# Performance work log

Hardware: AMD Instinct MI355X
Metric: run time of the kernel (lower is better)

## Reference

```python
import jax, jax.numpy as jnp
import numpy as np

N_NODES = 100000
N_EDGES = 1600000
N_GRAPHS = 64
HID = 128
N_EXPERTS = 8
IN_DIM = 4


def setup_inputs() -> dict:
    key = jax.random.key(0)
    ks = jax.random.split(key, 12)
    atomic_numbers = jax.random.uniform(ks[0], (N_NODES,), dtype=jnp.float32) * 80.0
    pos = jax.random.normal(ks[1], (N_NODES, 3), dtype=jnp.float32)
    edge_index = jax.random.randint(ks[2], (2, N_EDGES), 0, N_NODES, dtype=jnp.int64)
    batch = jnp.sort(jax.random.randint(ks[3], (N_NODES,), 0, N_GRAPHS, dtype=jnp.int64))
    s1 = 1.0 / np.sqrt(IN_DIM)
    s2 = 1.0 / np.sqrt(HID)
    W1 = jax.random.uniform(ks[4], (IN_DIM, HID), jnp.float32, -s1, s1)
    b1 = jnp.zeros((HID,), jnp.float32)
    W2 = jax.random.uniform(ks[5], (HID, HID), jnp.float32, -s2, s2)
    b2 = jnp.zeros((HID,), jnp.float32)
    Wlin = jax.random.uniform(ks[6], (HID, N_EXPERTS), jnp.float32, -s2, s2)
    blin = jax.random.uniform(ks[7], (N_EXPERTS,), jnp.float32, -s2, s2)
    return {"atomic_numbers": atomic_numbers, "pos": pos, "edge_index": edge_index,
            "batch": batch, "W1": W1, "b1": b1, "W2": W2, "b2": b2,
            "Wlin": Wlin, "blin": blin}


def _gcn_conv(x, W, b, src, dst, deg_inv_sqrt, n_nodes):
    # PyG GCNConv: x' = W x; aggregate deg^-1/2[src]*deg^-1/2[dst] * x'[src] into dst; + bias
    h = x @ W  # [N, out]
    norm = deg_inv_sqrt[src] * deg_inv_sqrt[dst]  # [E+N]
    msg = h[src] * norm[:, None]  # gathered, normalized messages
    out = jax.ops.segment_sum(msg, dst, num_segments=n_nodes)
    return out + b


def reference(atomic_numbers, pos, edge_index, batch, W1, b1, W2, b2, Wlin, blin):
    n = atomic_numbers.shape[0]
    x = jnp.concatenate([atomic_numbers[:, None], pos], axis=-1)  # [N, 4]
    # add self-loops (GCNConv default add_self_loops=True)
    loop = jnp.arange(n, dtype=edge_index.dtype)
    src = jnp.concatenate([edge_index[0], loop])
    dst = jnp.concatenate([edge_index[1], loop])
    deg = jax.ops.segment_sum(jnp.ones_like(dst, dtype=jnp.float32), dst, num_segments=n)
    deg_inv_sqrt = jnp.where(deg > 0, jax.lax.rsqrt(jnp.maximum(deg, 1e-12)), 0.0)
    x = _gcn_conv(x, W1, b1, src, dst, deg_inv_sqrt, n)
    x = jax.nn.relu(x)
    # dropout p=0.5 is identity in eval mode
    x = _gcn_conv(x, W2, b2, src, dst, deg_inv_sqrt, n)
    x = x @ Wlin + blin  # [N, num_experts]
    # global_mean_pool over graph ids
    sums = jax.ops.segment_sum(x, batch, num_segments=N_GRAPHS)
    cnts = jax.ops.segment_sum(jnp.ones((n,), jnp.float32), batch, num_segments=N_GRAPHS)
    pooled = sums / jnp.maximum(cnts, 1.0)[:, None]
    return jax.nn.log_softmax(pooled, axis=1)
```

## Files before the change

### kernel.cpp

```cpp
#include <hip/hip_runtime.h>
#include <math.h>

#define HID 128
#define NEXP 8
#define NGRAPH 64
#define EPC 6144
#define MAXB 512
#define NXC 8
#define NREP 8
#define NPS 8
#define HALF 128

__device__ inline unsigned short f2bf(float f) {
    unsigned u = __float_as_uint(f);
    u += 0x7FFF + ((u >> 16) & 1);
    return (unsigned short)(u >> 16);
}
__device__ inline unsigned packbf(float lo, float hi) {
    return (unsigned)f2bf(lo) | ((unsigned)f2bf(hi) << 16);
}
__device__ inline float bflo(unsigned u) { return __uint_as_float(u << 16); }
__device__ inline float bfhi(unsigned u) { return __uint_as_float(u & 0xFFFF0000u); }

__global__ void k_init0(float* __restrict__ pool, float* __restrict__ pcnt,
                        const float* __restrict__ W2, const float* __restrict__ Wlin,
                        const float* __restrict__ b2, float* __restrict__ C,
                        float* __restrict__ bb2, int* __restrict__ gcur8,
                        int mregions, int capx) {
    int i = blockIdx.x * 256 + threadIdx.x;
    if (i < mregions) gcur8[i] = i * capx;
    if (i < NREP * NGRAPH * NEXP) pool[i] = 0.0f;
    if (i < NREP * NGRAPH) pcnt[i] = 0.0f;
    int ci = i - NREP * NGRAPH * NEXP;
    if (ci >= 0 && ci < HID * NEXP) {
        int k = ci >> 3, j = ci & 7;
        float s = 0.0f;
        for (int m = 0; m < HID; m++) s += W2[k * HID + m] * Wlin[m * NEXP + j];
        C[ci] = s;
    }
    int bi = ci - HID * NEXP;
    if (bi >= 0 && bi < NEXP) {
        float s = 0.0f;
        for (int m = 0; m < HID; m++) s += b2[m] * Wlin[m * NEXP + bi];
        bb2[bi] = s;
    }
}

__global__ void __launch_bounds__(256) k_binA(
        const int* __restrict__ src, const int* __restrict__ dst,
        int* __restrict__ gcur8, unsigned* __restrict__ binned, int e, int nbuck) {
    __shared__ int h0[MAXB];
    __shared__ int h1[MAXB];
    __shared__ int lstart[MAXB];
    __shared__ int lcur[MAXB];
    __shared__ int gbase[MAXB];
    __shared__ int wtot[4];
    __shared__ unsigned packed[EPC];
    __shared__ unsigned short sbkt[EPC];
    int c = blockIdx.x, t = threadIdx.x;
    int w = t >> 6, lane = t & 63;
    int x = c & (NXC - 1);
    int start = c * EPC;
    int m = e - start < EPC ? e - start : EPC;

    int d[24], sv[24];
    if (m == EPC) {
        const int4* d4 = (const int4*)(dst + start);
        const int4* s4 = (const int4*)(src + start);
#pragma unroll
        for (int q = 0; q < 6; q++) {
            int4 dd4 = d4[6 * t + q];
            int4 ss4 = s4[6 * t + q];
            d[4 * q + 0] = dd4.x; d[4 * q + 1] = dd4.y;
            d[4 * q + 2] = dd4.z; d[4 * q + 3] = dd4.w;
            sv[4 * q + 0] = ss4.x; sv[4 * q + 1] = ss4.y;
            sv[4 * q + 2] = ss4.z; sv[4 * q + 3] = ss4.w;
        }
    } else {
#pragma unroll
        for (int j = 0; j < 24; j++) {
            int idx = t * 24 + j;
            if (idx < m) { d[j] = dst[start + idx]; sv[j] = src[start + idx]; }
        }
    }
    int* hm = (w < 2) ? h0 : h1;
    h0[t] = 0; h0[t + 256] = 0;
    h1[t] = 0; h1[t + 256] = 0;
    __syncthreads();
#pragma unroll
    for (int j = 0; j < 24; j++)
        if (t * 24 + j < m) atomicAdd(&hm[d[j] >> 8], 1);
    __syncthreads();
    int v0 = h0[2 * t] + h1[2 * t];
    int v1 = h0[2 * t + 1] + h1[2 * t + 1];
    int sum = v0 + v1;
    int incl = sum;
#pragma unroll
    for (int dd = 1; dd < 64; dd <<= 1) {
        int y = __shfl_up(incl, dd, 64);
        if (lane >= dd) incl += y;
    }
    if (lane == 63) wtot[w] = incl;
    __syncthreads();
    int pre = 0;
#pragma unroll
    for (int ww = 0; ww < 4; ww++) pre += (ww < w) ? wtot[ww] : 0;
    int ex = pre + incl - sum;
    lstart[2 * t] = ex;     lstart[2 * t + 1] = ex + v0;
    lcur[2 * t]   = ex;     lcur[2 * t + 1]   = ex + v0;
    for (int b = t; b < nbuck; b += 256) {
        int hv = h0[b] + h1[b];
        gbase[b] = hv ? atomicAdd(&gcur8[b * NXC + x], hv) : 0;
    }
    __syncthreads();
#pragma unroll
    for (int j = 0; j < 24; j++) {
        if (t * 24 + j < m) {
            int b = d[j] >> 8;
            int p = atomicAdd(&lcur[b], 1);
            packed[p] = ((unsigned)(d[j] & 255) << 24) | (unsigned)sv[j];
            sbkt[p] = (unsigned short)b;
        }
    }
    __syncthreads();
    for (int idx = t; idx < m; idx += 256) {
        int b = sbkt[idx];
        binned[gbase[b] + (idx - lstart[b])] = packed[idx];
    }
}

__global__ void k_binB(const unsigned* __restrict__ binned, const int* __restrict__ gcur8,
                       const float* __restrict__ an, const float* __restrict__ pos,
                       int* __restrict__ cnt, int* __restrict__ off,
                       float* __restrict__ dinv, float4* __restrict__ xs,
                       int* __restrict__ eidx, int n, int capx) {
    __shared__ int h[HALF];
    __shared__ int cur[HALF];
    __shared__ int wtot[2];
    int bh = blockIdx.x, t = threadIdx.x;
    int b = bh >> 1, half = bh & 1;
    int cbase = b * NXC;
    int hb = cbase * capx + half * (NXC / 2) * capx;
    if (t < HALF) h[t] = 0;
    __syncthreads();
#pragma unroll
    for (int x = 0; x < NXC; x++) {
        int rs = (cbase + x) * capx, re = gcur8[cbase + x];
        for (int k = rs + t; k < re; k += 256) {
            int f = (int)(binned[k] >> 24);
            if ((f >> 7) == half) atomicAdd(&h[f & (HALF - 1)], 1);
        }
    }
    __syncthreads();
    int v = 0, ex = 0;
    if (t < HALF) {
        int lane = t & 63, w = t >> 6;
        v = h[t];
        int incl = v;
#pragma unroll
        for (int dd = 1; dd < 64; dd <<= 1) {
            int y = __shfl_up(incl, dd, 64);
            if (lane >= dd) incl += y;
        }
        if (lane == 63) wtot[w] = incl;
        ex = incl - v;
    }
    __syncthreads();
    if (t < HALF) {
        if (t >= 64) ex += wtot[0];
        cur[t] = ex;
        int node = (b << 8) + half * HALF + t;
        if (node < n) {
            float di = rsqrtf((float)v + 1.0f);
            cnt[node]  = v;
            off[node]  = hb + ex;
            dinv[node] = di;
            xs[node] = make_float4(an[node] * di, pos[3 * node] * di,
                                   pos[3 * node + 1] * di, pos[3 * node + 2] * di);
        }
    }
    __syncthreads();
#pragma unroll
    for (int x = 0; x < NXC; x++) {
        int rs = (cbase + x) * capx, re = gcur8[cbase + x];
        for (int k = rs + t; k < re; k += 256) {
            unsigned u = binned[k];
            int f = (int)(u >> 24);
            if ((f >> 7) == half) {
                int p = atomicAdd(&cur[f & (HALF - 1)], 1);
                eidx[hb + p] = (int)(u & 0xFFFFFF);
            }
        }
    }
}

__global__ void k_gxz(const float4* __restrict__ xs, const int* __restrict__ eidx,
                      const int* __restrict__ off, const int* __restrict__ cnt,
                      const float* __restrict__ dinv, const float* __restrict__ W1,
                      const float* __restrict__ b1, const float* __restrict__ C,
                      uint4* __restrict__ z, int n) {
    int tid = blockIdx.x * 256 + threadIdx.x;
    int i = tid >> 1;
    int par = tid & 1;
    if (i >= n) return;
    float4 a = par ? make_float4(0.f, 0.f, 0.f, 0.f) : xs[i];
    int o = off[i], c = cnt[i];
    int k = par;
    for (; k + 6 < c; k += 8) {
        int i0 = eidx[o + k],     i1 = eidx[o + k + 2];
        int i2 = eidx[o + k + 4], i3 = eidx[o + k + 6];
        float4 v0 = xs[i0], v1 = xs[i1], v2 = xs[i2], v3 = xs[i3];
        a.x += v0.x + v1.x + v2.x + v3.x;
        a.y += v0.y + v1.y + v2.y + v3.y;
        a.z += v0.z + v1.z + v2.z + v3.z;
        a.w += v0.w + v1.w + v2.w + v3.w;
    }
    for (; k < c; k += 2) {
        float4 v0 = xs[eidx[o + k]];
        a.x += v0.x; a.y += v0.y; a.z += v0.z; a.w += v0.w;
    }
    a.x += __shfl_xor(a.x, 1, 64);
    a.y += __shfl_xor(a.y, 1, 64);
    a.z += __shfl_xor(a.z, 1, 64);
    a.w += __shfl_xor(a.w, 1, 64);
    float di = dinv[i];
    float z0 = 0.f, z1 = 0.f, z2 = 0.f, z3 = 0.f,
          z4 = 0.f, z5 = 0.f, z6 = 0.f, z7 = 0.f;
#pragma unroll 4
    for (int kk = 0; kk < HID; kk++) {
        float x1k = fmaxf(di * (a.x * W1[kk] + a.y * W1[HID + kk] +
                                a.z * W1[2 * HID + kk] + a.w * W1[3 * HID + kk])
                          + b1[kk], 0.0f);
        const float* cr = C + kk * NEXP;
        z0 += x1k * cr[0]; z1 += x1k * cr[1];
        z2 += x1k * cr[2]; z3 += x1k * cr[3];
        z4 += x1k * cr[4]; z5 += x1k * cr[5];
        z6 += x1k * cr[6]; z7 += x1k * cr[7];
    }
    if (par == 0) {
        uint4 outv;
        outv.x = packbf(z0 * di, z1 * di);
        outv.y = packbf(z2 * di, z3 * di);
        outv.z = packbf(z4 * di, z5 * di);
        outv.w = packbf(z6 * di, z7 * di);
        z[i] = outv;
    }
}

__global__ void k_gz(const uint4* __restrict__ z4, const int* __restrict__ eidx,
                     const int* __restrict__ off, const int* __restrict__ cnt,
                     const float* __restrict__ dinv, const int* __restrict__ batch,
                     float* __restrict__ pool, float* __restrict__ pcnt, int n) {
    int t = threadIdx.x;
    int slot = t >> 4;
    int l = t & 15;
    int i0 = blockIdx.x * (16 * NPS) + slot * NPS;
    if (i0 >= n) return;
    int i1 = i0 + NPS < n ? i0 + NPS : n;
    int rep = (blockIdx.x + slot) & (NREP - 1);
    float* rp  = pool + (size_t)rep * NGRAPH * NEXP;
    float* rpc = pcnt + (size_t)rep * NGRAPH;
    int Q = l >> 2;

    int curg = -1;
    float r0 = 0.0f, r1 = 0.0f, runlen = 0.0f;
    for (int i = i0; i < i1; i++) {
        float a0 = 0.f, a1 = 0.f, a2 = 0.f, a3 = 0.f,
              a4 = 0.f, a5 = 0.f, a6 = 0.f, a7 = 0.f;
        int o = off[i], c = cnt[i];
        for (int k = l; k < c; k += 16) {
            uint4 zr = z4[eidx[o + k]];
            a0 += bflo(zr.x); a1 += bfhi(zr.x);
            a2 += bflo(zr.y); a3 += bfhi(zr.y);
            a4 += bflo(zr.z); a5 += bfhi(zr.z);
            a6 += bflo(zr.w); a7 += bfhi(zr.w);
        }
        if (l == 0) {
            uint4 zr = z4[i];
            a0 += bflo(zr.x); a1 += bfhi(zr.x);
            a2 += bflo(zr.y); a3 += bfhi(zr.y);
            a4 += bflo(zr.z); a5 += bfhi(zr.z);
            a6 += bflo(zr.w); a7 += bfhi(zr.w);
        }
        a0 += __shfl_xor(a0, 8, 64); a1 += __shfl_xor(a1, 8, 64);
        a2 += __shfl_xor(a2, 8, 64); a3 += __shfl_xor(a3, 8, 64);
        a4 += __shfl_xor(a4, 8, 64); a5 += __shfl_xor(a5, 8, 64);
        a6 += __shfl_xor(a6, 8, 64); a7 += __shfl_xor(a7, 8, 64);
        a0 += __shfl_xor(a0, 4, 64); a1 += __shfl_xor(a1, 4, 64);
        a2 += __shfl_xor(a2, 4, 64); a3 += __shfl_xor(a3, 4, 64);
        a4 += __shfl_xor(a4, 4, 64); a5 += __shfl_xor(a5, 4, 64);
        a6 += __shfl_xor(a6, 4, 64); a7 += __shfl_xor(a7, 4, 64);
        float r0v, r1v;
        switch (Q) {
            case 0:  r0v = a0; r1v = a1; break;
            case 1:  r0v = a2; r1v = a3; break;
            case 2:  r0v = a4; r1v = a5; break;
            default: r0v = a6; r1v = a7; break;
        }
        r0v += __shfl_xor(r0v, 1, 64); r1v += __shfl_xor(r1v, 1, 64);
        r0v += __shfl_xor(r0v, 2, 64); r1v += __shfl_xor(r1v, 2, 64);
        float di = dinv[i];
        float v0 = di * r0v, v1 = di * r1v;
        int g = batch[i];
        if (g != curg) {
            if (curg >= 0 && (l & 3) == 0) {
                atomicAdd(&rp[curg * NEXP + 2 * Q], r0);
                atomicAdd(&rp[curg * NEXP + 2 * Q + 1], r1);
                if (l == 0) atomicAdd(&rpc[curg], runlen);
            }
            curg = g; r0 = v0; r1 = v1; runlen = 1.0f;
        } else { r0 += v0; r1 += v1; runlen += 1.0f; }
    }
    if (curg >= 0 && (l & 3) == 0) {
        atomicAdd(&rp[curg * NEXP + 2 * Q], r0);
        atomicAdd(&rp[curg * NEXP + 2 * Q + 1], r1);
        if (l == 0) atomicAdd(&rpc[curg], runlen);
    }
}

__global__ void k_lsm(const float* __restrict__ pool, const float* __restrict__ pcnt,
                      const float* __restrict__ blin, const float* __restrict__ bb2,
                      float* __restrict__ out) {
    int g = threadIdx.x;
    if (g >= NGRAPH) return;
    float p[NEXP];
#pragma unroll
    for (int k = 0; k < NEXP; k++) p[k] = 0.0f;
    float cg = 0.0f;
#pragma unroll
    for (int rr = 0; rr < NREP; rr++) {
#pragma unroll
        for (int k = 0; k < NEXP; k++) p[k] += pool[rr * NGRAPH * NEXP + g * NEXP + k];
        cg += pcnt[rr * NGRAPH + g];
    }
    float inv = 1.0f / fmaxf(cg, 1.0f);
    float v[NEXP], m = -1e30f;
#pragma unroll
    for (int k = 0; k < NEXP; k++) {
        v[k] = p[k] * inv + blin[k] + bb2[k];
        m = fmaxf(m, v[k]);
    }
    float s = 0.0f;
#pragma unroll
    for (int k = 0; k < NEXP; k++) s += expf(v[k] - m);
    float ls = logf(s);
#pragma unroll
    for (int k = 0; k < NEXP; k++) out[g * NEXP + k] = v[k] - m - ls;
}

extern "C" void kernel_launch(void* const* d_in, const int* in_sizes, int n_in,
                              void* d_out, int out_size, void* d_ws, size_t ws_size,
                              hipStream_t stream) {
    const float* an   = (const float*)d_in[0];
    const float* pos  = (const float*)d_in[1];
    const int*   ei   = (const int*)d_in[2];
    const int*   batch= (const int*)d_in[3];
    const float* W1   = (const float*)d_in[4];
    const float* b1   = (const float*)d_in[5];
    const float* W2   = (const float*)d_in[6];
    const float* b2   = (const float*)d_in[7];
    const float* Wlin = (const float*)d_in[8];
    const float* blin = (const float*)d_in[9];
    float* out = (float*)d_out;

    const int n = in_sizes[0];
    const int e = in_sizes[2] / 2;
    const int* src = ei;
    const int* dst = ei + e;

    const int nbuck = (n + 255) >> 8;
    const int ch    = (e + EPC - 1) / EPC;
    const int mreg  = nbuck * NXC;
    const int capx  = 2 * (e / (mreg > 0 ? mreg : 1)) + 256;

    char* p = (char*)d_ws;
    float4* xs    = (float4*)p;       p += sizeof(float4) * (size_t)n;
    uint4*  z     = (uint4*)p;        p += sizeof(uint4) * (size_t)n;
    float* C      = (float*)p;        p += sizeof(float) * HID * NEXP;
    float* bb2    = (float*)p;        p += sizeof(float) * NEXP;
    float* dinv   = (float*)p;        p += sizeof(float) * (size_t)n;
    float* pool   = (float*)p;        p += sizeof(float) * NREP * NGRAPH * NEXP;
    float* pcnt   = (float*)p;        p += sizeof(float) * NREP * NGRAPH;
    int*   cnt    = (int*)p;          p += sizeof(int) * (size_t)n;
    int*   off    = (int*)p;          p += sizeof(int) * (size_t)n;
    int*   gcur8  = (int*)p;          p += sizeof(int) * (mreg + 8);
    unsigned* binned = (unsigned*)p;  p += sizeof(unsigned) * (size_t)mreg * capx;
    int*   eidx   = (int*)p;          p += sizeof(int) * (size_t)mreg * capx;

    const int initN = NREP * NGRAPH * NEXP + HID * NEXP + NEXP;
    const int initG = initN > mreg ? initN : mreg;
    k_init0<<<(initG + 255) / 256, 256, 0, stream>>>(pool, pcnt, W2, Wlin, b2, C,
                                                     bb2, gcur8, mreg, capx);
    k_binA<<<ch, 256, 0, stream>>>(src, dst, gcur8, binned, e, nbuck);
    k_binB<<<2 * nbuck, 256, 0, stream>>>(binned, gcur8, an, pos, cnt, off, dinv,
                                          xs, eidx, n, capx);

    k_gxz<<<(2 * n + 255) / 256, 256, 0, stream>>>(xs, eidx, off, cnt, dinv,
                                                   W1, b1, C, z, n);

    k_gz<<<(n + 16 * NPS - 1) / (16 * NPS), 256, 0, stream>>>(z, eidx, off, cnt, dinv,
                                                              batch, pool, pcnt, n);
    k_lsm<<<1, 64, 0, stream>>>(pool, pcnt, blin, bb2, out);
}
```

Before: 175.8 us.

## Stage binB edges in LDS, shrink binA chunk, fuse log-softmax into gather kernel

Three separate changes. The binA edge chunk per block drops from 6144 to 2048, which launches more blocks. k_binB now reads the binned region once, compacts the edges of its half into shared-memory staging with a wave ballot, and scatters from there instead of reading global memory twice. The final log-softmax moves into the last block of k_gz through an atomic ticket, removing one kernel launch. The staging buffer has a fixed cap of 4096, so any edges beyond it would be silently dropped.

```diff
diff --git a/kernel.cpp b/kernel.cpp
--- a/kernel.cpp
+++ b/kernel.cpp
@@ -4,12 +4,14 @@
 #define HID 128
 #define NEXP 8
 #define NGRAPH 64
-#define EPC 6144
+#define EPC 2048
+#define EPT 8
 #define MAXB 512
 #define NXC 8
 #define NREP 8
 #define NPS 8
 #define HALF 128
+#define STAGE_CAP 4096
 
 __device__ inline unsigned short f2bf(float f) {
     unsigned u = __float_as_uint(f);
@@ -29,6 +31,7 @@
                         int mregions, int capx) {
     int i = blockIdx.x * 256 + threadIdx.x;
     if (i < mregions) gcur8[i] = i * capx;
+    if (i == mregions) gcur8[i] = 0;
     if (i < NREP * NGRAPH * NEXP) pool[i] = 0.0f;
     if (i < NREP * NGRAPH) pcnt[i] = 0.0f;
     int ci = i - NREP * NGRAPH * NEXP;
@@ -63,14 +66,14 @@
     int start = c * EPC;
     int m = e - start < EPC ? e - start : EPC;
 
-    int d[24], sv[24];
+    int d[EPT], sv[EPT];
     if (m == EPC) {
         const int4* d4 = (const int4*)(dst + start);
         const int4* s4 = (const int4*)(src + start);
 #pragma unroll
-        for (int q = 0; q < 6; q++) {
-            int4 dd4 = d4[6 * t + q];
-            int4 ss4 = s4[6 * t + q];
+        for (int q = 0; q < EPT / 4; q++) {
+            int4 dd4 = d4[(EPT / 4) * t + q];
+            int4 ss4 = s4[(EPT / 4) * t + q];
             d[4 * q + 0] = dd4.x; d[4 * q + 1] = dd4.y;
             d[4 * q + 2] = dd4.z; d[4 * q + 3] = dd4.w;
             sv[4 * q + 0] = ss4.x; sv[4 * q + 1] = ss4.y;
@@ -78,8 +81,8 @@
         }
     } else {
 #pragma unroll
-        for (int j = 0; j < 24; j++) {
-            int idx = t * 24 + j;
+        for (int j = 0; j < EPT; j++) {
+            int idx = t * EPT + j;
             if (idx < m) { d[j] = dst[start + idx]; sv[j] = src[start + idx]; }
         }
     }
@@ -88,8 +91,8 @@
     h1[t] = 0; h1[t + 256] = 0;
     __syncthreads();
 #pragma unroll
-    for (int j = 0; j < 24; j++)
-        if (t * 24 + j < m) atomicAdd(&hm[d[j] >> 8], 1);
+    for (int j = 0; j < EPT; j++)
+        if (t * EPT + j < m) atomicAdd(&hm[d[j] >> 8], 1);
     __syncthreads();
     int v0 = h0[2 * t] + h1[2 * t];
     int v1 = h0[2 * t + 1] + h1[2 * t + 1];
@@ -114,8 +117,8 @@
     }
     __syncthreads();
 #pragma unroll
-    for (int j = 0; j < 24; j++) {
-        if (t * 24 + j < m) {
+    for (int j = 0; j < EPT; j++) {
+        if (t * EPT + j < m) {
             int b = d[j] >> 8;
             int p = atomicAdd(&lcur[b], 1);
             packed[p] = ((unsigned)(d[j] & 255) << 24) | (unsigned)sv[j];
@@ -137,24 +140,44 @@
     __shared__ int h[HALF];
     __shared__ int cur[HALF];
     __shared__ int wtot[2];
+    __shared__ int scnt;
+    __shared__ unsigned stage[STAGE_CAP];
     int bh = blockIdx.x, t = threadIdx.x;
     int b = bh >> 1, half = bh & 1;
     int cbase = b * NXC;
     int hb = cbase * capx + half * (NXC / 2) * capx;
+    int lane = t & 63;
     if (t < HALF) h[t] = 0;
+    if (t == 0) scnt = 0;
     __syncthreads();
 #pragma unroll
     for (int x = 0; x < NXC; x++) {
         int rs = (cbase + x) * capx, re = gcur8[cbase + x];
-        for (int k = rs + t; k < re; k += 256) {
-            int f = (int)(binned[k] >> 24);
-            if ((f >> 7) == half) atomicAdd(&h[f & (HALF - 1)], 1);
+        for (int k0 = rs; k0 < re; k0 += 256) {
+            int k = k0 + t;
+            unsigned u = 0;
+            bool keep = false;
+            if (k < re) {
+                u = binned[k];
+                keep = ((int)(u >> 24) >> 7) == half;
+            }
+            unsigned long long msk = __ballot(keep);
+            int pre = __popcll(msk & ((1ull << lane) - 1ull));
+            int cw = __popcll(msk);
+            int base = 0;
+            if (lane == 0 && cw) base = atomicAdd(&scnt, cw);
+            base = __shfl(base, 0, 64);
+            if (keep) {
+                int p = base + pre;
+                if (p < STAGE_CAP) stage[p] = u;
+                atomicAdd(&h[(u >> 24) & (HALF - 1)], 1);
+            }
         }
     }
     __syncthreads();
     int v = 0, ex = 0;
     if (t < HALF) {
-        int lane = t & 63, w = t >> 6;
+        int w = t >> 6;
         v = h[t];
         int incl = v;
 #pragma unroll
@@ -180,17 +203,11 @@
         }
     }
     __syncthreads();
-#pragma unroll
-    for (int x = 0; x < NXC; x++) {
-        int rs = (cbase + x) * capx, re = gcur8[cbase + x];
-        for (int k = rs + t; k < re; k += 256) {
-            unsigned u = binned[k];
-            int f = (int)(u >> 24);
-            if ((f >> 7) == half) {
-                int p = atomicAdd(&cur[f & (HALF - 1)], 1);
-                eidx[hb + p] = (int)(u & 0xFFFFFF);
-            }
-        }
+    int total = scnt < STAGE_CAP ? scnt : STAGE_CAP;
+    for (int k = t; k < total; k += 256) {
+        unsigned u = stage[k];
+        int p = atomicAdd(&cur[(u >> 24) & (HALF - 1)], 1);
+        eidx[hb + p] = (int)(u & 0xFFFFFF);
     }
 }
 
@@ -250,102 +267,110 @@
 __global__ void k_gz(const uint4* __restrict__ z4, const int* __restrict__ eidx,
                      const int* __restrict__ off, const int* __restrict__ cnt,
                      const float* __restrict__ dinv, const int* __restrict__ batch,
-                     float* __restrict__ pool, float* __restrict__ pcnt, int n) {
+                     float* __restrict__ pool, float* __restrict__ pcnt,
+                     const float* __restrict__ blin, const float* __restrict__ bb2,
+                     float* __restrict__ out, int* __restrict__ ticket,
+                     int nblk, int n) {
     int t = threadIdx.x;
     int slot = t >> 4;
     int l = t & 15;
     int i0 = blockIdx.x * (16 * NPS) + slot * NPS;
-    if (i0 >= n) return;
-    int i1 = i0 + NPS < n ? i0 + NPS : n;
-    int rep = (blockIdx.x + slot) & (NREP - 1);
-    float* rp  = pool + (size_t)rep * NGRAPH * NEXP;
-    float* rpc = pcnt + (size_t)rep * NGRAPH;
-    int Q = l >> 2;
-
-    int curg = -1;
-    float r0 = 0.0f, r1 = 0.0f, runlen = 0.0f;
-    for (int i = i0; i < i1; i++) {
-        float a0 = 0.f, a1 = 0.f, a2 = 0.f, a3 = 0.f,
-              a4 = 0.f, a5 = 0.f, a6 = 0.f, a7 = 0.f;
-        int o = off[i], c = cnt[i];
-        for (int k = l; k < c; k += 16) {
-            uint4 zr = z4[eidx[o + k]];
-            a0 += bflo(zr.x); a1 += bfhi(zr.x);
-            a2 += bflo(zr.y); a3 += bfhi(zr.y);
-            a4 += bflo(zr.z); a5 += bfhi(zr.z);
-            a6 += bflo(zr.w); a7 += bfhi(zr.w);
-        }
-        if (l == 0) {
-            uint4 zr = z4[i];
-            a0 += bflo(zr.x); a1 += bfhi(zr.x);
-            a2 += bflo(zr.y); a3 += bfhi(zr.y);
-            a4 += bflo(zr.z); a5 += bfhi(zr.z);
-            a6 += bflo(zr.w); a7 += bfhi(zr.w);
-        }
-        a0 += __shfl_xor(a0, 8, 64); a1 += __shfl_xor(a1, 8, 64);
-        a2 += __shfl_xor(a2, 8, 64); a3 += __shfl_xor(a3, 8, 64);
-        a4 += __shfl_xor(a4, 8, 64); a5 += __shfl_xor(a5, 8, 64);
-        a6 += __shfl_xor(a6, 8, 64); a7 += __shfl_xor(a7, 8, 64);
-        a0 += __shfl_xor(a0, 4, 64); a1 += __shfl_xor(a1, 4, 64);
-        a2 += __shfl_xor(a2, 4, 64); a3 += __shfl_xor(a3, 4, 64);
-        a4 += __shfl_xor(a4, 4, 64); a5 += __shfl_xor(a5, 4, 64);
-        a6 += __shfl_xor(a6, 4, 64); a7 += __shfl_xor(a7, 4, 64);
-        float r0v, r1v;
-        switch (Q) {
-            case 0:  r0v = a0; r1v = a1; break;
-            case 1:  r0v = a2; r1v = a3; break;
-            case 2:  r0v = a4; r1v = a5; break;
-            default: r0v = a6; r1v = a7; break;
-        }
-        r0v += __shfl_xor(r0v, 1, 64); r1v += __shfl_xor(r1v, 1, 64);
-        r0v += __shfl_xor(r0v, 2, 64); r1v += __shfl_xor(r1v, 2, 64);
-        float di = dinv[i];
-        float v0 = di * r0v, v1 = di * r1v;
-        int g = batch[i];
-        if (g != curg) {
-            if (curg >= 0 && (l & 3) == 0) {
-                atomicAdd(&rp[curg * NEXP + 2 * Q], r0);
-                atomicAdd(&rp[curg * NEXP + 2 * Q + 1], r1);
-                if (l == 0) atomicAdd(&rpc[curg], runlen);
+    if (i0 < n) {
+        int i1 = i0 + NPS < n ? i0 + NPS : n;
+        int rep = (blockIdx.x + slot) & (NREP - 1);
+        float* rp  = pool + (size_t)rep * NGRAPH * NEXP;
+        float* rpc = pcnt + (size_t)rep * NGRAPH;
+        int Q = l >> 2;
+
+        int curg = -1;
+        float r0 = 0.0f, r1 = 0.0f, runlen = 0.0f;
+        for (int i = i0; i < i1; i++) {
+            float a0 = 0.f, a1 = 0.f, a2 = 0.f, a3 = 0.f,
+                  a4 = 0.f, a5 = 0.f, a6 = 0.f, a7 = 0.f;
+            int o = off[i], c = cnt[i];
+            for (int k = l; k < c; k += 16) {
+                uint4 zr = z4[eidx[o + k]];
+                a0 += bflo(zr.x); a1 += bfhi(zr.x);
+                a2 += bflo(zr.y); a3 += bfhi(zr.y);
+                a4 += bflo(zr.z); a5 += bfhi(zr.z);
+                a6 += bflo(zr.w); a7 += bfhi(zr.w);
             }
-            curg = g; r0 = v0; r1 = v1; runlen = 1.0f;
-        } else { r0 += v0; r1 += v1; runlen += 1.0f; }
-    }
-    if (curg >= 0 && (l & 3) == 0) {
-        atomicAdd(&rp[curg * NEXP + 2 * Q], r0);
-        atomicAdd(&rp[curg * NEXP + 2 * Q + 1], r1);
-        if (l == 0) atomicAdd(&rpc[curg], runlen);
-    }
-}
-
-__global__ void k_lsm(const float* __restrict__ pool, const float* __restrict__ pcnt,
-                      const float* __restrict__ blin, const float* __restrict__ bb2,
-                      float* __restrict__ out) {
-    int g = threadIdx.x;
-    if (g >= NGRAPH) return;
-    float p[NEXP];
-#pragma unroll
-    for (int k = 0; k < NEXP; k++) p[k] = 0.0f;
-    float cg = 0.0f;
-#pragma unroll
-    for (int rr = 0; rr < NREP; rr++) {
-#pragma unroll
-        for (int k = 0; k < NEXP; k++) p[k] += pool[rr * NGRAPH * NEXP + g * NEXP + k];
-        cg += pcnt[rr * NGRAPH + g];
-    }
-    float inv = 1.0f / fmaxf(cg, 1.0f);
-    float v[NEXP], m = -1e30f;
-#pragma unroll
-    for (int k = 0; k < NEXP; k++) {
-        v[k] = p[k] * inv + blin[k] + bb2[k];
-        m = fmaxf(m, v[k]);
-    }
-    float s = 0.0f;
-#pragma unroll
-    for (int k = 0; k < NEXP; k++) s += expf(v[k] - m);
-    float ls = logf(s);
-#pragma unroll
-    for (int k = 0; k < NEXP; k++) out[g * NEXP + k] = v[k] - m - ls;
+            if (l == 0) {
+                uint4 zr = z4[i];
+                a0 += bflo(zr.x); a1 += bfhi(zr.x);
+                a2 += bflo(zr.y); a3 += bfhi(zr.y);
+                a4 += bflo(zr.z); a5 += bfhi(zr.z);
+                a6 += bflo(zr.w); a7 += bfhi(zr.w);
+            }
+            a0 += __shfl_xor(a0, 8, 64); a1 += __shfl_xor(a1, 8, 64);
+            a2 += __shfl_xor(a2, 8, 64); a3 += __shfl_xor(a3, 8, 64);
+            a4 += __shfl_xor(a4, 8, 64); a5 += __shfl_xor(a5, 8, 64);
+            a6 += __shfl_xor(a6, 8, 64); a7 += __shfl_xor(a7, 8, 64);
+            a0 += __shfl_xor(a0, 4, 64); a1 += __shfl_xor(a1, 4, 64);
+            a2 += __shfl_xor(a2, 4, 64); a3 += __shfl_xor(a3, 4, 64);
+            a4 += __shfl_xor(a4, 4, 64); a5 += __shfl_xor(a5, 4, 64);
+            a6 += __shfl_xor(a6, 4, 64); a7 += __shfl_xor(a7, 4, 64);
+            float r0v, r1v;
+            switch (Q) {
+                case 0:  r0v = a0; r1v = a1; break;
+                case 1:  r0v = a2; r1v = a3; break;
+                case 2:  r0v = a4; r1v = a5; break;
+                default: r0v = a6; r1v = a7; break;
+            }
+            r0v += __shfl_xor(r0v, 1, 64); r1v += __shfl_xor(r1v, 1, 64);
+            r0v += __shfl_xor(r0v, 2, 64); r1v += __shfl_xor(r1v, 2, 64);
+            float di = dinv[i];
+            float v0 = di * r0v, v1 = di * r1v;
+            int g = batch[i];
+            if (g != curg) {
+                if (curg >= 0 && (l & 3) == 0) {
+                    atomicAdd(&rp[curg * NEXP + 2 * Q], r0);
+                    atomicAdd(&rp[curg * NEXP + 2 * Q + 1], r1);
+                    if (l == 0) atomicAdd(&rpc[curg], runlen);
+                }
+                curg = g; r0 = v0; r1 = v1; runlen = 1.0f;
+            } else { r0 += v0; r1 += v1; runlen += 1.0f; }
+        }
+        if (curg >= 0 && (l & 3) == 0) {
+            atomicAdd(&rp[curg * NEXP + 2 * Q], r0);
+            atomicAdd(&rp[curg * NEXP + 2 * Q + 1], r1);
+            if (l == 0) atomicAdd(&rpc[curg], runlen);
+        }
+    }
+    __shared__ int lastFlag;
+    __syncthreads();
+    if (t == 0) {
+        __threadfence();
+        lastFlag = (atomicAdd(ticket, 1) == nblk - 1);
+    }
+    __syncthreads();
+    if (lastFlag && t < NGRAPH) {
+        int g = t;
+        float p[NEXP];
+#pragma unroll
+        for (int k = 0; k < NEXP; k++) p[k] = 0.0f;
+        float cg = 0.0f;
+#pragma unroll
+        for (int rr = 0; rr < NREP; rr++) {
+#pragma unroll
+            for (int k = 0; k < NEXP; k++)
+                p[k] += atomicAdd(&pool[rr * NGRAPH * NEXP + g * NEXP + k], 0.0f);
+            cg += atomicAdd(&pcnt[rr * NGRAPH + g], 0.0f);
+        }
+        float inv = 1.0f / fmaxf(cg, 1.0f);
+        float v[NEXP], m = -1e30f;
+#pragma unroll
+        for (int k = 0; k < NEXP; k++) {
+            v[k] = p[k] * inv + blin[k] + bb2[k];
+            m = fmaxf(m, v[k]);
+        }
+        float s = 0.0f;
+#pragma unroll
+        for (int k = 0; k < NEXP; k++) s += expf(v[k] - m);
+        float ls = logf(s);
+#pragma unroll
+        for (int k = 0; k < NEXP; k++) out[g * NEXP + k] = v[k] - m - ls;
+    }
 }
 
 extern "C" void kernel_launch(void* const* d_in, const int* in_sizes, int n_in,
@@ -386,9 +411,10 @@
     int*   gcur8  = (int*)p;          p += sizeof(int) * (mreg + 8);
     unsigned* binned = (unsigned*)p;  p += sizeof(unsigned) * (size_t)mreg * capx;
     int*   eidx   = (int*)p;          p += sizeof(int) * (size_t)mreg * capx;
+    int*   ticket = gcur8 + mreg;
 
     const int initN = NREP * NGRAPH * NEXP + HID * NEXP + NEXP;
-    const int initG = initN > mreg ? initN : mreg;
+    const int initG = initN > mreg + 1 ? initN : mreg + 1;
     k_init0<<<(initG + 255) / 256, 256, 0, stream>>>(pool, pcnt, W2, Wlin, b2, C,
                                                      bb2, gcur8, mreg, capx);
     k_binA<<<ch, 256, 0, stream>>>(src, dst, gcur8, binned, e, nbuck);
@@ -398,7 +424,7 @@
     k_gxz<<<(2 * n + 255) / 256, 256, 0, stream>>>(xs, eidx, off, cnt, dinv,
                                                    W1, b1, C, z, n);
 
-    k_gz<<<(n + 16 * NPS - 1) / (16 * NPS), 256, 0, stream>>>(z, eidx, off, cnt, dinv,
-                                                              batch, pool, pcnt, n);
-    k_lsm<<<1, 64, 0, stream>>>(pool, pcnt, blin, bb2, out);
-}
+    const int nblk = (n + 16 * NPS - 1) / (16 * NPS);
+    k_gz<<<nblk, 256, 0, stream>>>(z, eidx, off, cnt, dinv, batch, pool, pcnt,
+                                   blin, bb2, out, ticket, nblk, n);
+}
```

Measured after the change: 206.2 us. 1.17x slower.
